# Performance work log

Hardware: AMD Instinct MI355X
Metric: run time of the kernel (lower is better)

The kernel has to match this reference:

```python
import jax, jax.numpy as jnp
import numpy as np
from jax import lax

N_LAYER = 4
D_MODEL = 512
N_HEAD = 8
D_HEAD = 64
D_INNER = 2048
KERNEL = 9
POOL = 8
N_CLASSES = 10
BATCH = 4
RAW_LEN = 8192


def setup_inputs() -> dict:
    key = jax.random.key(0)
    ks = jax.random.split(key, 12)
    s = 0.02
    return {
        "signal": jax.random.normal(ks[0], (BATCH, RAW_LEN), jnp.float32),
        "conv_w": jax.random.normal(ks[1], (KERNEL, 1, D_MODEL), jnp.float32) * s,
        "conv_b": jnp.zeros((D_MODEL,), jnp.float32),
        "qkv_w": jax.random.normal(ks[2], (N_LAYER, D_MODEL, 3 * N_HEAD * D_HEAD), jnp.float32) * s,
        "r_w": jax.random.normal(ks[3], (N_LAYER, D_MODEL, N_HEAD * D_HEAD), jnp.float32) * s,
        "o_w": jax.random.normal(ks[4], (N_LAYER, N_HEAD * D_HEAD, D_MODEL), jnp.float32) * s,
        "ff1_w": jax.random.normal(ks[5], (N_LAYER, D_MODEL, D_INNER), jnp.float32) * s,
        "ff1_b": jnp.zeros((N_LAYER, D_INNER), jnp.float32),
        "ff2_w": jax.random.normal(ks[6], (N_LAYER, D_INNER, D_MODEL), jnp.float32) * s,
        "ff2_b": jnp.zeros((N_LAYER, D_MODEL), jnp.float32),
        "r_w_bias": jax.random.normal(ks[7], (N_HEAD, D_HEAD), jnp.float32) * s,
        "r_r_bias": jax.random.normal(ks[8], (N_HEAD, D_HEAD), jnp.float32) * s,
        "fc_w": jax.random.normal(ks[9], (D_MODEL, N_CLASSES), jnp.float32) * s,
        "fc_b": jnp.zeros((N_CLASSES,), jnp.float32),
    }


def _rel_shift(x):
    # x: [qlen, rlen, bsz, n_head]; TF-XL pad/reshape/slice trick
    q, r, b, n = x.shape
    x = jnp.pad(x, ((0, 0), (1, 0), (0, 0), (0, 0)))
    x = x.reshape(r + 1, q, b, n)[1:]
    return x.reshape(q, r, b, n)


def _forward(signal, conv_w, conv_b, qkv_w, r_w, o_w, ff1_w, ff1_b, ff2_w,
             ff2_b, r_w_bias, r_r_bias, fc_w, fc_b):
    # Conv1D (valid) -> ReLU -> AveragePooling1D
    x = signal[:, :, None]  # [B, L, 1]
    x = lax.conv_general_dilated(x, conv_w, (1,), 'VALID',
                                 dimension_numbers=('NWC', 'WIO', 'NWC')) + conv_b
    x = jax.nn.relu(x)
    B, Lp, D = x.shape
    S = Lp // POOL  # Lp is divisible by POOL for our sizes (keras valid pooling)
    x = x[:, :S * POOL].reshape(B, S, POOL, D).mean(axis=2)
    core = x.transpose(1, 0, 2)  # [S, B, D]

    # sinusoidal relative positional embedding, pos_seq = S-1 .. -(S-1)
    pos_seq = jnp.arange(S - 1, -S, -1, dtype=core.dtype)  # [2S-1]
    inv_freq = 1.0 / (10000.0 ** (jnp.arange(0, D, 2, dtype=core.dtype) / D))
    sin_inp = pos_seq[:, None] * inv_freq[None, :]
    pos_emb = jnp.concatenate([jnp.sin(sin_inp), jnp.cos(sin_inp)], -1)  # [2S-1, D]

    scale = 1.0 / np.sqrt(D_HEAD).astype(np.float32)
    for l in range(N_LAYER):
        heads = core @ qkv_w[l]  # [S, B, 3*H*Dh]
        q, k, v = jnp.split(heads, 3, axis=-1)
        q = q.reshape(S, B, N_HEAD, D_HEAD)
        k = k.reshape(S, B, N_HEAD, D_HEAD)
        v = v.reshape(S, B, N_HEAD, D_HEAD)
        rk = (pos_emb @ r_w[l]).reshape(2 * S - 1, N_HEAD, D_HEAD)

        AC = jnp.einsum('ibnd,jbnd->ijbn', q + r_w_bias, k)      # content term
        BD = jnp.einsum('ibnd,jnd->ijbn', q + r_r_bias, rk)      # position term
        BD = _rel_shift(BD)[:, :S]                                # [S, S, B, H]
        attn_prob = jax.nn.softmax((AC + BD) * scale, axis=1)
        attn_vec = jnp.einsum('ijbn,jbnd->ibnd', attn_prob, v)
        attn_out = attn_vec.reshape(S, B, N_HEAD * D_HEAD) @ o_w[l]
        core = core + attn_out

        # position-wise FF with residual
        h = jax.nn.relu(core @ ff1_w[l] + ff1_b[l]) @ ff2_w[l] + ff2_b[l]
        core = core + h

    # classification head on last timestep
    return core[-1] @ fc_w + fc_b  # [B, n_classes]


def reference(signal, conv_w, conv_b, qkv_w, r_w, o_w, ff1_w, ff1_b, ff2_w,
              ff2_b, r_w_bias, r_r_bias, fc_w, fc_b):
    return _forward(signal, conv_w, conv_b, qkv_w, r_w, o_w, ff1_w, ff1_b,
                    ff2_w, ff2_b, r_w_bias, r_r_bias, fc_w, fc_b)
```

## Files before the change

### kernel.cpp

```cpp
#include <hip/hip_runtime.h>
#include <math.h>

#define S_LEN   1023
#define BATCH_N 4
#define DMODEL  512
#define NHEAD   8
#define DHEAD   64
#define DINNER  2048
#define NLAYER  4
#define RAWLEN  8192
#define POOLW   8
#define KERNW   9
#define RLEN    (2*S_LEN-1)
#define MROWS   (S_LEN*BATCH_N)

using bf16x8 = __attribute__((ext_vector_type(8))) short;
using f32x4  = __attribute__((ext_vector_type(4))) float;

__device__ __forceinline__ unsigned short f2bf(float f) {
    union { float f; unsigned int u; } v; v.f = f;
    unsigned int u = v.u;
    return (unsigned short)((u + 0x7fffu + ((u >> 16) & 1u)) >> 16);
}
__device__ __forceinline__ float bf2f(unsigned short h) {
    union { unsigned int u; float f; } v; v.u = ((unsigned int)h) << 16;
    return v.f;
}

__device__ __forceinline__ void gload_lds16(const void* g, void* l) {
    using gvoid = const __attribute__((address_space(1))) void;
    using lvoid = __attribute__((address_space(3))) void;
    gvoid* gp = reinterpret_cast<gvoid*>(reinterpret_cast<unsigned long long>(g));
    lvoid* lp = reinterpret_cast<lvoid*>((unsigned int)reinterpret_cast<unsigned long long>(l));
    __builtin_amdgcn_global_load_lds(gp, lp, 16, 0, 0);
}

__global__ __launch_bounds__(512) void conv_pool_kernel(
    const float* __restrict__ sig, const float* __restrict__ cw,
    const float* __restrict__ cb, float* __restrict__ core,
    unsigned short* __restrict__ core_bf)
{
    int s = blockIdx.x, b = blockIdx.y, d = threadIdx.x;
    __shared__ float sseg[POOLW + KERNW - 1];
    if (d < POOLW + KERNW - 1) sseg[d] = sig[b*RAWLEN + s*POOLW + d];
    __syncthreads();
    float w[KERNW];
#pragma unroll
    for (int k = 0; k < KERNW; k++) w[k] = cw[k*DMODEL + d];
    float bias = cb[d];
    float acc = 0.f;
#pragma unroll
    for (int p = 0; p < POOLW; p++) {
        float c = bias;
#pragma unroll
        for (int k = 0; k < KERNW; k++) c = fmaf(sseg[p+k], w[k], c);
        acc += fmaxf(c, 0.f);
    }
    float v = acc * (1.0f/POOLW);
    core[(s*BATCH_N + b)*DMODEL + d] = v;
    core_bf[(s*BATCH_N + b)*DMODEL + d] = f2bf(v);
}

__global__ __launch_bounds__(512) void posemb_kernel(unsigned short* __restrict__ pe)
{
    int j = blockIdx.x, d = threadIdx.x;
    float pos = (float)(S_LEN - 1 - j);
    int i = (d < 256) ? d : d - 256;
    float invf = exp2f(-(float)i * (13.287712f/256.0f));
    float a = pos * invf;
    pe[j*DMODEL + d] = f2bf((d < 256) ? __sinf(a) : __cosf(a));
}

__global__ __launch_bounds__(256) void transpose_all_kernel(
    const float* __restrict__ qw, const float* __restrict__ rw,
    const float* __restrict__ ow, const float* __restrict__ f1,
    const float* __restrict__ f2,
    unsigned short* __restrict__ qT, unsigned short* __restrict__ rT,
    unsigned short* __restrict__ oT, unsigned short* __restrict__ f1T,
    unsigned short* __restrict__ f2T)
{
    int id = blockIdx.x;
    const float* W; unsigned short* Wt; int K, N, bx, by;
    if (id < 768)       { W = qw;  Wt = qT;  K = 512;  N = 1536; bx = id % 48; by = id / 48; }
    else if (id < 1024) { id -= 768;  W = rw;  Wt = rT;  K = 512;  N = 512;  bx = id % 16; by = id / 16; }
    else if (id < 1280) { id -= 1024; W = ow;  Wt = oT;  K = 512;  N = 512;  bx = id % 16; by = id / 16; }
    else if (id < 2304) { id -= 1280; W = f1;  Wt = f1T; K = 512;  N = 2048; bx = id % 64; by = id / 64; }
    else                { id -= 2304; W = f2;  Wt = f2T; K = 2048; N = 512;  bx = id % 16; by = id / 16; }

    __shared__ float L[32][33];
    int n0 = bx*32, k0 = by*32;
    int t = threadIdx.x;
    int kk = t>>3, nq = (t&7)*4;
    float4 v = *reinterpret_cast<const float4*>(&W[(size_t)(k0+kk)*N + n0 + nq]);
    L[kk][nq+0]=v.x; L[kk][nq+1]=v.y; L[kk][nq+2]=v.z; L[kk][nq+3]=v.w;
    __syncthreads();
    int nn = t>>3, kq = (t&7)*4;
    ushort4 o;
    o.x = f2bf(L[kq+0][nn]); o.y = f2bf(L[kq+1][nn]);
    o.z = f2bf(L[kq+2][nn]); o.w = f2bf(L[kq+3][nn]);
    *reinterpret_cast<ushort4*>(&Wt[(size_t)(n0+nn)*K + k0 + kq]) = o;
}

template<int BN, bool ACCUM, bool BIAS, bool RELU, bool WF32, bool WBF>
__global__ __launch_bounds__(256) void gemm_mfma(
    const unsigned short* __restrict__ A, const unsigned short* __restrict__ Bt,
    const float* __restrict__ bias, float* __restrict__ C,
    unsigned short* __restrict__ Cb, int M, int N, int K)
{
    constexpr int MF = (BN == 128) ? 4 : 2;
    __shared__ unsigned short As[128*32];
    __shared__ unsigned short Bs[BN*32];
    int bm = blockIdx.y * 128, bn = blockIdx.x * BN;
    int tid = threadIdx.x, lane = tid & 63, wid = tid >> 6;

    f32x4 acc[MF][4];
#pragma unroll
    for (int m=0;m<MF;m++)
#pragma unroll
        for (int n=0;n<4;n++) acc[m][n] = (f32x4){0.f,0.f,0.f,0.f};

    int r0 = wid*16 + (lane>>2);
    int slot = (lane&3)*8;
    int ga0 = bm + r0;      if (ga0 > M-1) ga0 = M-1;
    int ga1 = bm + r0 + 64; if (ga1 > M-1) ga1 = M-1;
    const unsigned short* pA0 = A  + (size_t)ga0*K + slot;
    const unsigned short* pA1 = A  + (size_t)ga1*K + slot;
    const unsigned short* pB0 = Bt + (size_t)(bn + r0)*K + slot;
    const unsigned short* pB1 = (BN==128) ? Bt + (size_t)(bn + r0 + 64)*K + slot : nullptr;
    char* lA0 = (char*)As + wid*1024;
    char* lA1 = (char*)As + (wid+4)*1024;
    char* lB0 = (char*)Bs + wid*1024;
    char* lB1 = (char*)Bs + (wid+4)*1024;

    int ar = (BN==128 ? (wid>>1)*64 : wid*32) + (lane&15);
    int br = (BN==128 ? (wid&1)*64 : 0) + (lane&15);
    int kc = (lane>>4)*8;

    for (int k0 = 0; k0 < K; k0 += 32) {
        __syncthreads();
        gload_lds16(pA0, lA0);
        gload_lds16(pA1, lA1);
        gload_lds16(pB0, lB0);
        if (BN == 128) gload_lds16(pB1, lB1);
        pA0 += 32; pA1 += 32; pB0 += 32; if (BN==128) pB1 += 32;
        __syncthreads();
        bf16x8 a[MF], b[4];
#pragma unroll
        for (int m=0;m<MF;m++) a[m] = *reinterpret_cast<const bf16x8*>(&As[(ar + m*16)*32 + kc]);
#pragma unroll
        for (int n=0;n<4;n++) b[n] = *reinterpret_cast<const bf16x8*>(&Bs[(br + n*16)*32 + kc]);
#pragma unroll
        for (int m=0;m<MF;m++)
#pragma unroll
            for (int n=0;n<4;n++)
                acc[m][n] = __builtin_amdgcn_mfma_f32_16x16x32_bf16(a[m], b[n], acc[m][n], 0,0,0);
    }

    int col0 = bn + (BN==128 ? (wid&1)*64 : 0) + (lane&15);
    int rbase = bm + (BN==128 ? (wid>>1)*64 : wid*32) + (lane>>4)*4;
#pragma unroll
    for (int m=0;m<MF;m++) {
#pragma unroll
        for (int n=0;n<4;n++) {
            int col = col0 + n*16;
            float bv = BIAS ? bias[col] : 0.f;
#pragma unroll
            for (int r=0;r<4;r++) {
                int row = rbase + m*16 + r;
                if (row < M) {
                    float v = acc[m][n][r] + bv;
                    if (RELU) v = fmaxf(v, 0.f);
                    size_t off = (size_t)row*N + col;
                    if (ACCUM) v += C[off];
                    if (WF32) C[off] = v;
                    if (WBF)  Cb[off] = f2bf(v);
                }
            }
        }
    }
}

template<bool ACCUM, bool BIAS, bool RELU, bool WF32, bool WBF>
__global__ __launch_bounds__(256) void gemm_mfma64(
    const unsigned short* __restrict__ A, const unsigned short* __restrict__ Bt,
    const float* __restrict__ bias, float* __restrict__ C,
    unsigned short* __restrict__ Cb, int M, int N, int K)
{
    __shared__ unsigned short As[64*32];
    __shared__ unsigned short Bs[64*32];
    int bm = blockIdx.y * 64, bn = blockIdx.x * 64;
    int tid = threadIdx.x, lane = tid & 63, wid = tid >> 6;
    int wr = wid >> 1, wc = wid & 1;

    f32x4 acc[2][2];
#pragma unroll
    for (int m=0;m<2;m++)
#pragma unroll
        for (int n=0;n<2;n++) acc[m][n] = (f32x4){0.f,0.f,0.f,0.f};

    int r0 = wid*16 + (lane>>2);
    int slot = (lane&3)*8;
    int ga = bm + r0; if (ga > M-1) ga = M-1;
    const unsigned short* pA = A  + (size_t)ga*K + slot;
    const unsigned short* pB = Bt + (size_t)(bn + r0)*K + slot;
    char* lA = (char*)As + wid*1024;
    char* lB = (char*)Bs + wid*1024;

    int ar = wr*32 + (lane&15);
    int br = wc*32 + (lane&15);
    int kc = (lane>>4)*8;

    for (int k0 = 0; k0 < K; k0 += 32) {
        __syncthreads();
        gload_lds16(pA, lA);
        gload_lds16(pB, lB);
        pA += 32; pB += 32;
        __syncthreads();
        bf16x8 a[2], b[2];
#pragma unroll
        for (int m=0;m<2;m++) a[m] = *reinterpret_cast<const bf16x8*>(&As[(ar + m*16)*32 + kc]);
#pragma unroll
        for (int n=0;n<2;n++) b[n] = *reinterpret_cast<const bf16x8*>(&Bs[(br + n*16)*32 + kc]);
#pragma unroll
        for (int m=0;m<2;m++)
#pragma unroll
            for (int n=0;n<2;n++)
                acc[m][n] = __builtin_amdgcn_mfma_f32_16x16x32_bf16(a[m], b[n], acc[m][n], 0,0,0);
    }

    int col0 = bn + wc*32 + (lane&15);
    int rbase = bm + wr*32 + (lane>>4)*4;
#pragma unroll
    for (int m=0;m<2;m++) {
#pragma unroll
        for (int n=0;n<2;n++) {
            int col = col0 + n*16;
            float bv = BIAS ? bias[col] : 0.f;
#pragma unroll
            for (int r=0;r<4;r++) {
                int row = rbase + m*16 + r;
                if (row < M) {
                    float v = acc[m][n][r] + bv;
                    if (RELU) v = fmaxf(v, 0.f);
                    size_t off = (size_t)row*N + col;
                    if (ACCUM) v += C[off];
                    if (WF32) C[off] = v;
                    if (WBF)  Cb[off] = f2bf(v);
                }
            }
        }
    }
}

#define TI 32
#define TJ 32
#define PSTR 40
#define ACSTR 36
#define BDSTR 68

__global__ __launch_bounds__(256) void attn_mfma_kernel(
    const unsigned short* __restrict__ heads,
    const unsigned short* __restrict__ rk,
    const float* __restrict__ rwb, const float* __restrict__ rrb,
    unsigned short* __restrict__ av)
{
    int i0 = blockIdx.x * TI;
    int bn = blockIdx.y; int b = bn >> 3, n = bn & 7;
    int tid = threadIdx.x, lane = tid & 63, wid = tid >> 6;
    int mi = wid >> 1;
    int half = wid & 1;
    int kc = (lane>>4)*8;
    int l15 = lane & 15;

    __shared__ float Sac[TI*ACSTR];
    __shared__ float Sbd[TI*BDSTR];
    __shared__ unsigned short Pb[TI*PSTR];
    __shared__ float mrow[TI], lrow[TI], frow[TI];

    const int base0 = (S_LEN-1) - i0 - (TI-1);

    bf16x8 qwf0, qwf1, qrf0, qrf1;
    {
        int gi = i0 + mi*16 + l15; if (gi > S_LEN-1) gi = S_LEN-1;
        const unsigned short* qb = heads + (size_t)(gi*BATCH_N + b)*1536 + n*64;
        bf16x8 u0 = *reinterpret_cast<const bf16x8*>(qb + kc);
        bf16x8 u1 = *reinterpret_cast<const bf16x8*>(qb + 32 + kc);
#pragma unroll
        for (int e=0;e<8;e++) {
            float f0 = bf2f((unsigned short)u0[e]);
            float f1 = bf2f((unsigned short)u1[e]);
            qwf0[e] = (short)f2bf(f0 + rwb[n*64 + kc + e]);
            qrf0[e] = (short)f2bf(f0 + rrb[n*64 + kc + e]);
            qwf1[e] = (short)f2bf(f1 + rwb[n*64 + 32 + kc + e]);
            qrf1[e] = (short)f2bf(f1 + rrb[n*64 + 32 + kc + e]);
        }
    }
    if (tid < TI) { mrow[tid] = -1e30f; lrow[tid] = 0.f; }

    f32x4 Oa[2];
    Oa[0] = (f32x4){0.f,0.f,0.f,0.f};
    Oa[1] = (f32x4){0.f,0.f,0.f,0.f};

    int rw = mi*16 + (lane>>4)*4;

    for (int t = 0; t < 32; t++) {
        int j0 = t * TJ;
        __syncthreads();

        {
            int gj = j0 + half*16 + l15; if (gj > S_LEN-1) gj = S_LEN-1;
            const unsigned short* kb = heads + (size_t)(gj*BATCH_N + b)*1536 + 512 + n*64;
            bf16x8 kf0 = *reinterpret_cast<const bf16x8*>(kb + kc);
            bf16x8 kf1 = *reinterpret_cast<const bf16x8*>(kb + 32 + kc);
            f32x4 s = (f32x4){0.f,0.f,0.f,0.f};
            s = __builtin_amdgcn_mfma_f32_16x16x32_bf16(qwf0, kf0, s, 0,0,0);
            s = __builtin_amdgcn_mfma_f32_16x16x32_bf16(qwf1, kf1, s, 0,0,0);
            int ci = half*16 + l15;
#pragma unroll
            for (int r=0;r<4;r++) Sac[(rw+r)*ACSTR + ci] = s[r];
        }
        if (t == 0) {
#pragma unroll
            for (int nn=0;nn<2;nn++) {
                int w = (half*2+nn)*16 + l15;
                int gr = base0 + w; gr = gr < 0 ? 0 : (gr > RLEN-1 ? RLEN-1 : gr);
                const unsigned short* rb = rk + (size_t)gr*DMODEL + n*64;
                bf16x8 rf0 = *reinterpret_cast<const bf16x8*>(rb + kc);
                bf16x8 rf1 = *reinterpret_cast<const bf16x8*>(rb + 32 + kc);
                f32x4 sb = (f32x4){0.f,0.f,0.f,0.f};
                sb = __builtin_amdgcn_mfma_f32_16x16x32_bf16(qrf0, rf0, sb, 0,0,0);
                sb = __builtin_amdgcn_mfma_f32_16x16x32_bf16(qrf1, rf1, sb, 0,0,0);
#pragma unroll
                for (int r=0;r<4;r++) Sbd[(rw+r)*BDSTR + w] = sb[r];
            }
        } else {
            int pblk = ((t & 1) ? 0 : 2) + half;
            int w = pblk*16 + l15;
            int off = 32*(t+1) + (w & 31);
            int gr = base0 + off; gr = gr < 0 ? 0 : (gr > RLEN-1 ? RLEN-1 : gr);
            const unsigned short* rb = rk + (size_t)gr*DMODEL + n*64;
            bf16x8 rf0 = *reinterpret_cast<const bf16x8*>(rb + kc);
            bf16x8 rf1 = *reinterpret_cast<const bf16x8*>(rb + 32 + kc);
            f32x4 sb = (f32x4){0.f,0.f,0.f,0.f};
            sb = __builtin_amdgcn_mfma_f32_16x16x32_bf16(qrf0, rf0, sb, 0,0,0);
            sb = __builtin_amdgcn_mfma_f32_16x16x32_bf16(qrf1, rf1, sb, 0,0,0);
#pragma unroll
            for (int r=0;r<4;r++) Sbd[(rw+r)*BDSTR + w] = sb[r];
        }
        __syncthreads();

        {
            int r = tid>>3, seg = tid&7, jl = seg*4;
            float4 ac = *reinterpret_cast<const float4*>(&Sac[r*ACSTR + jl]);
            int cbase = 32*t + (TI-1) - r;
            float s0 = (ac.x + Sbd[r*BDSTR + ((cbase+jl+0)&63)]) * 0.125f;
            float s1 = (ac.y + Sbd[r*BDSTR + ((cbase+jl+1)&63)]) * 0.125f;
            float s2 = (ac.z + Sbd[r*BDSTR + ((cbase+jl+2)&63)]) * 0.125f;
            float s3 = (ac.w + Sbd[r*BDSTR + ((cbase+jl+3)&63)]) * 0.125f;
            int jg = j0 + jl;
            if (jg+0 >= S_LEN) s0 = -1e30f;
            if (jg+1 >= S_LEN) s1 = -1e30f;
            if (jg+2 >= S_LEN) s2 = -1e30f;
            if (jg+3 >= S_LEN) s3 = -1e30f;
            float tm = fmaxf(fmaxf(s0,s1), fmaxf(s2,s3));
            tm = fmaxf(tm, __shfl_xor(tm, 1));
            tm = fmaxf(tm, __shfl_xor(tm, 2));
            tm = fmaxf(tm, __shfl_xor(tm, 4));
            float mo = mrow[r];
            float mnew = fmaxf(mo, tm);
            float f = __expf(mo - mnew);
            float e0 = __expf(s0 - mnew), e1 = __expf(s1 - mnew);
            float e2 = __expf(s2 - mnew), e3 = __expf(s3 - mnew);
            float ssum = e0+e1+e2+e3;
            ssum += __shfl_xor(ssum, 1);
            ssum += __shfl_xor(ssum, 2);
            ssum += __shfl_xor(ssum, 4);
            if (seg == 0) {
                mrow[r] = mnew;
                lrow[r] = lrow[r]*f + ssum;
                frow[r] = f;
            }
            ushort4 pw;
            pw.x = f2bf(e0); pw.y = f2bf(e1); pw.z = f2bf(e2); pw.w = f2bf(e3);
            *reinterpret_cast<ushort4*>(&Pb[r*PSTR + jl]) = pw;
        }
        __syncthreads();

        {
            float f0 = frow[rw+0], f1 = frow[rw+1], f2 = frow[rw+2], f3 = frow[rw+3];
#pragma unroll
            for (int nn=0;nn<2;nn++) {
                Oa[nn][0] *= f0; Oa[nn][1] *= f1; Oa[nn][2] *= f2; Oa[nn][3] *= f3;
            }
            bf16x8 pf = *reinterpret_cast<const bf16x8*>(&Pb[(mi*16 + l15)*PSTR + kc]);
            const unsigned short* vb = heads + 1024 + n*64;
#pragma unroll
            for (int nn=0;nn<2;nn++) {
                int d = (half*2+nn)*16 + l15;
                bf16x8 vf;
#pragma unroll
                for (int e=0;e<8;e++) {
                    int gj = j0 + kc + e; if (gj > S_LEN-1) gj = S_LEN-1;
                    vf[e] = (short)vb[(size_t)(gj*BATCH_N + b)*1536 + d];
                }
                Oa[nn] = __builtin_amdgcn_mfma_f32_16x16x32_bf16(pf, vf, Oa[nn], 0,0,0);
            }
        }
    }
    __syncthreads();

    {
        float linv[4];
#pragma unroll
        for (int r=0;r<4;r++) linv[r] = 1.0f / lrow[rw+r];
#pragma unroll
        for (int nn=0;nn<2;nn++) {
            int d = (half*2+nn)*16 + l15;
#pragma unroll
            for (int r=0;r<4;r++) {
                int gi = i0 + rw + r;
                if (gi < S_LEN)
                    av[(size_t)(gi*BATCH_N + b)*DMODEL + n*64 + d] = f2bf(Oa[nn][r]*linv[r]);
            }
        }
    }
}

__global__ __launch_bounds__(64) void final_kernel(
    const float* __restrict__ core, const float* __restrict__ fcw,
    const float* __restrict__ fcb, float* __restrict__ out)
{
    int idx = blockIdx.x;
    int b = idx / 10, c = idx % 10;
    int lane = threadIdx.x;
    const float* row = &core[(size_t)((S_LEN-1)*BATCH_N + b)*DMODEL];
    float acc = 0.f;
    for (int d = lane; d < DMODEL; d += 64)
        acc = fmaf(row[d], fcw[d*10 + c], acc);
#pragma unroll
    for (int off = 32; off; off >>= 1) acc += __shfl_xor(acc, off);
    if (lane == 0) out[b*10 + c] = acc + fcb[c];
}

extern "C" void kernel_launch(void* const* d_in, const int* in_sizes, int n_in,
                              void* d_out, int out_size, void* d_ws, size_t ws_size,
                              hipStream_t stream)
{
    const float* sig   = (const float*)d_in[0];
    const float* cw    = (const float*)d_in[1];
    const float* cb    = (const float*)d_in[2];
    const float* qkv_w = (const float*)d_in[3];
    const float* r_w   = (const float*)d_in[4];
    const float* o_w   = (const float*)d_in[5];
    const float* ff1_w = (const float*)d_in[6];
    const float* ff1_b = (const float*)d_in[7];
    const float* ff2_w = (const float*)d_in[8];
    const float* ff2_b = (const float*)d_in[9];
    const float* rwb   = (const float*)d_in[10];
    const float* rrb   = (const float*)d_in[11];
    const float* fcw   = (const float*)d_in[12];
    const float* fcb   = (const float*)d_in[13];
    float* out = (float*)d_out;

    float* core = (float*)d_ws;
    unsigned short* core_bf = (unsigned short*)(core + (size_t)MROWS*DMODEL);
    unsigned short* pe_bf   = core_bf + (size_t)MROWS*DMODEL;
    unsigned short* rk_bf   = pe_bf   + (size_t)RLEN*DMODEL;
    unsigned short* av_bf   = rk_bf   + (size_t)RLEN*DMODEL;
    unsigned short* big_bf  = av_bf   + (size_t)MROWS*DMODEL;
    unsigned short* qkvT = big_bf + (size_t)MROWS*DINNER;
    unsigned short* rwT  = qkvT + (size_t)(3*DMODEL)*DMODEL;
    unsigned short* owT  = rwT  + (size_t)DMODEL*DMODEL;
    unsigned short* ff1T = owT  + (size_t)DMODEL*DMODEL;
    unsigned short* ff2T = ff1T + (size_t)DINNER*DMODEL;

    conv_pool_kernel<<<dim3(S_LEN, BATCH_N), 512, 0, stream>>>(sig, cw, cb, core, core_bf);
    posemb_kernel<<<RLEN, 512, 0, stream>>>(pe_bf);

    for (int l = 0; l < NLAYER; l++) {
        transpose_all_kernel<<<3328, 256, 0, stream>>>(
            qkv_w + (size_t)l*DMODEL*(3*DMODEL),
            r_w   + (size_t)l*DMODEL*DMODEL,
            o_w   + (size_t)l*DMODEL*DMODEL,
            ff1_w + (size_t)l*DMODEL*DINNER,
            ff2_w + (size_t)l*DINNER*DMODEL,
            qkvT, rwT, owT, ff1T, ff2T);

        gemm_mfma<64,false,false,false,false,true><<<dim3(24,32), 256, 0, stream>>>(
            core_bf, qkvT, nullptr, nullptr, big_bf, MROWS, 3*DMODEL, DMODEL);
        gemm_mfma64<false,false,false,false,true><<<dim3(8,32), 256, 0, stream>>>(
            pe_bf, rwT, nullptr, nullptr, rk_bf, RLEN, DMODEL, DMODEL);
        attn_mfma_kernel<<<dim3(32,32), 256, 0, stream>>>(big_bf, rk_bf, rwb, rrb, av_bf);
        gemm_mfma64<true,false,false,true,true><<<dim3(8,64), 256, 0, stream>>>(
            av_bf, owT, nullptr, core, core_bf, MROWS, DMODEL, DMODEL);
        gemm_mfma<128,false,true,true,false,true><<<dim3(16,32), 256, 0, stream>>>(
            core_bf, ff1T, ff1_b + (size_t)l*DINNER, nullptr, big_bf, MROWS, DINNER, DMODEL);
        gemm_mfma64<true,true,false,true,true><<<dim3(8,64), 256, 0, stream>>>(
            big_bf, ff2T, ff2_b + (size_t)l*DMODEL, core, core_bf, MROWS, DMODEL, DINNER);
    }

    final_kernel<<<40, 64, 0, stream>>>(core, fcw, fcb, out);
}
```

Before: 729.6 us.

## Double attention key tile width and prefetch V fragments before score phase

The attention kernel now processes 64 key columns per iteration instead of 32, halving the loop trip count and the number of block-wide barriers. The sliding BD window doubles to 128 entries, and the softmax step handles 8 scores per thread. V fragments are gathered from global memory at the top of each iteration, so their latency overlaps with the QK and QR MFMAs and the softmax. This raises register and LDS use per block, which may reduce occupancy.

New measurement: 752.6 us. 3.2% more time.

```diff
diff --git a/kernel.cpp b/kernel.cpp
--- a/kernel.cpp
+++ b/kernel.cpp
@@ -253,10 +253,10 @@
 }
 
 #define TI 32
-#define TJ 32
-#define PSTR 40
-#define ACSTR 36
-#define BDSTR 68
+#define TJ 64
+#define PSTR 72
+#define ACSTR 68
+#define BDSTR 132
 
 __global__ __launch_bounds__(256) void attn_mfma_kernel(
     const unsigned short* __restrict__ heads,
@@ -303,26 +303,45 @@
 
     int rw = mi*16 + (lane>>4)*4;
 
-    for (int t = 0; t < 32; t++) {
+    for (int t = 0; t < 16; t++) {
         int j0 = t * TJ;
         __syncthreads();
 
+        bf16x8 vpre[2][2];
         {
-            int gj = j0 + half*16 + l15; if (gj > S_LEN-1) gj = S_LEN-1;
+            const unsigned short* vb = heads + 1024 + n*64;
+#pragma unroll
+            for (int nn=0;nn<2;nn++) {
+                int d = (half + nn*2)*16 + l15;
+#pragma unroll
+                for (int h=0;h<2;h++) {
+#pragma unroll
+                    for (int e=0;e<8;e++) {
+                        int gj = j0 + h*32 + kc + e; if (gj > S_LEN-1) gj = S_LEN-1;
+                        vpre[nn][h][e] = (short)vb[(size_t)(gj*BATCH_N + b)*1536 + d];
+                    }
+                }
+            }
+        }
+
+#pragma unroll
+        for (int cc=0;cc<2;cc++) {
+            int cb = half + cc*2;
+            int gj = j0 + cb*16 + l15; if (gj > S_LEN-1) gj = S_LEN-1;
             const unsigned short* kb = heads + (size_t)(gj*BATCH_N + b)*1536 + 512 + n*64;
             bf16x8 kf0 = *reinterpret_cast<const bf16x8*>(kb + kc);
             bf16x8 kf1 = *reinterpret_cast<const bf16x8*>(kb + 32 + kc);
             f32x4 s = (f32x4){0.f,0.f,0.f,0.f};
             s = __builtin_amdgcn_mfma_f32_16x16x32_bf16(qwf0, kf0, s, 0,0,0);
             s = __builtin_amdgcn_mfma_f32_16x16x32_bf16(qwf1, kf1, s, 0,0,0);
-            int ci = half*16 + l15;
+            int ci = cb*16 + l15;
 #pragma unroll
             for (int r=0;r<4;r++) Sac[(rw+r)*ACSTR + ci] = s[r];
         }
         if (t == 0) {
 #pragma unroll
-            for (int nn=0;nn<2;nn++) {
-                int w = (half*2+nn)*16 + l15;
+            for (int q=0;q<4;q++) {
+                int w = (half + q*2)*16 + l15;
                 int gr = base0 + w; gr = gr < 0 ? 0 : (gr > RLEN-1 ? RLEN-1 : gr);
                 const unsigned short* rb = rk + (size_t)gr*DMODEL + n*64;
                 bf16x8 rf0 = *reinterpret_cast<const bf16x8*>(rb + kc);
@@ -334,44 +353,49 @@
                 for (int r=0;r<4;r++) Sbd[(rw+r)*BDSTR + w] = sb[r];
             }
         } else {
-            int pblk = ((t & 1) ? 0 : 2) + half;
-            int w = pblk*16 + l15;
-            int off = 32*(t+1) + (w & 31);
-            int gr = base0 + off; gr = gr < 0 ? 0 : (gr > RLEN-1 ? RLEN-1 : gr);
-            const unsigned short* rb = rk + (size_t)gr*DMODEL + n*64;
-            bf16x8 rf0 = *reinterpret_cast<const bf16x8*>(rb + kc);
-            bf16x8 rf1 = *reinterpret_cast<const bf16x8*>(rb + 32 + kc);
-            f32x4 sb = (f32x4){0.f,0.f,0.f,0.f};
-            sb = __builtin_amdgcn_mfma_f32_16x16x32_bf16(qrf0, rf0, sb, 0,0,0);
-            sb = __builtin_amdgcn_mfma_f32_16x16x32_bf16(qrf1, rf1, sb, 0,0,0);
-#pragma unroll
-            for (int r=0;r<4;r++) Sbd[(rw+r)*BDSTR + w] = sb[r];
+            int pbase = (t & 1) ? 0 : 4;
+#pragma unroll
+            for (int q=0;q<2;q++) {
+                int w = (pbase + half + q*2)*16 + l15;
+                int off = 64*(t+1) + (w & 63);
+                int gr = base0 + off; gr = gr < 0 ? 0 : (gr > RLEN-1 ? RLEN-1 : gr);
+                const unsigned short* rb = rk + (size_t)gr*DMODEL + n*64;
+                bf16x8 rf0 = *reinterpret_cast<const bf16x8*>(rb + kc);
+                bf16x8 rf1 = *reinterpret_cast<const bf16x8*>(rb + 32 + kc);
+                f32x4 sb = (f32x4){0.f,0.f,0.f,0.f};
+                sb = __builtin_amdgcn_mfma_f32_16x16x32_bf16(qrf0, rf0, sb, 0,0,0);
+                sb = __builtin_amdgcn_mfma_f32_16x16x32_bf16(qrf1, rf1, sb, 0,0,0);
+#pragma unroll
+                for (int r=0;r<4;r++) Sbd[(rw+r)*BDSTR + w] = sb[r];
+            }
         }
         __syncthreads();
 
         {
-            int r = tid>>3, seg = tid&7, jl = seg*4;
-            float4 ac = *reinterpret_cast<const float4*>(&Sac[r*ACSTR + jl]);
-            int cbase = 32*t + (TI-1) - r;
-            float s0 = (ac.x + Sbd[r*BDSTR + ((cbase+jl+0)&63)]) * 0.125f;
-            float s1 = (ac.y + Sbd[r*BDSTR + ((cbase+jl+1)&63)]) * 0.125f;
-            float s2 = (ac.z + Sbd[r*BDSTR + ((cbase+jl+2)&63)]) * 0.125f;
-            float s3 = (ac.w + Sbd[r*BDSTR + ((cbase+jl+3)&63)]) * 0.125f;
-            int jg = j0 + jl;
-            if (jg+0 >= S_LEN) s0 = -1e30f;
-            if (jg+1 >= S_LEN) s1 = -1e30f;
-            if (jg+2 >= S_LEN) s2 = -1e30f;
-            if (jg+3 >= S_LEN) s3 = -1e30f;
-            float tm = fmaxf(fmaxf(s0,s1), fmaxf(s2,s3));
+            int r = tid>>3, seg = tid&7, jl = seg*8;
+            int cbase = 64*t + (TI-1) - r;
+            float s[8];
+            float4 ac0 = *reinterpret_cast<const float4*>(&Sac[r*ACSTR + jl]);
+            float4 ac1 = *reinterpret_cast<const float4*>(&Sac[r*ACSTR + jl + 4]);
+            s[0]=ac0.x; s[1]=ac0.y; s[2]=ac0.z; s[3]=ac0.w;
+            s[4]=ac1.x; s[5]=ac1.y; s[6]=ac1.z; s[7]=ac1.w;
+#pragma unroll
+            for (int e=0;e<8;e++) {
+                s[e] = (s[e] + Sbd[r*BDSTR + ((cbase+jl+e)&127)]) * 0.125f;
+                if (j0 + jl + e >= S_LEN) s[e] = -1e30f;
+            }
+            float tm = s[0];
+#pragma unroll
+            for (int e=1;e<8;e++) tm = fmaxf(tm, s[e]);
             tm = fmaxf(tm, __shfl_xor(tm, 1));
             tm = fmaxf(tm, __shfl_xor(tm, 2));
             tm = fmaxf(tm, __shfl_xor(tm, 4));
             float mo = mrow[r];
             float mnew = fmaxf(mo, tm);
             float f = __expf(mo - mnew);
-            float e0 = __expf(s0 - mnew), e1 = __expf(s1 - mnew);
-            float e2 = __expf(s2 - mnew), e3 = __expf(s3 - mnew);
-            float ssum = e0+e1+e2+e3;
+            float e0[8], ssum = 0.f;
+#pragma unroll
+            for (int e=0;e<8;e++) { e0[e] = __expf(s[e] - mnew); ssum += e0[e]; }
             ssum += __shfl_xor(ssum, 1);
             ssum += __shfl_xor(ssum, 2);
             ssum += __shfl_xor(ssum, 4);
@@ -380,9 +404,11 @@
                 lrow[r] = lrow[r]*f + ssum;
                 frow[r] = f;
             }
-            ushort4 pw;
-            pw.x = f2bf(e0); pw.y = f2bf(e1); pw.z = f2bf(e2); pw.w = f2bf(e3);
-            *reinterpret_cast<ushort4*>(&Pb[r*PSTR + jl]) = pw;
+            ushort4 pw0, pw1;
+            pw0.x = f2bf(e0[0]); pw0.y = f2bf(e0[1]); pw0.z = f2bf(e0[2]); pw0.w = f2bf(e0[3]);
+            pw1.x = f2bf(e0[4]); pw1.y = f2bf(e0[5]); pw1.z = f2bf(e0[6]); pw1.w = f2bf(e0[7]);
+            *reinterpret_cast<ushort4*>(&Pb[r*PSTR + jl])     = pw0;
+            *reinterpret_cast<ushort4*>(&Pb[r*PSTR + jl + 4]) = pw1;
         }
         __syncthreads();
 
@@ -392,18 +418,12 @@
             for (int nn=0;nn<2;nn++) {
                 Oa[nn][0] *= f0; Oa[nn][1] *= f1; Oa[nn][2] *= f2; Oa[nn][3] *= f3;
             }
-            bf16x8 pf = *reinterpret_cast<const bf16x8*>(&Pb[(mi*16 + l15)*PSTR + kc]);
-            const unsigned short* vb = heads + 1024 + n*64;
+            bf16x8 pf0 = *reinterpret_cast<const bf16x8*>(&Pb[(mi*16 + l15)*PSTR + kc]);
+            bf16x8 pf1 = *reinterpret_cast<const bf16x8*>(&Pb[(mi*16 + l15)*PSTR + 32 + kc]);
 #pragma unroll
             for (int nn=0;nn<2;nn++) {
-                int d = (half*2+nn)*16 + l15;
-                bf16x8 vf;
-#pragma unroll
-                for (int e=0;e<8;e++) {
-                    int gj = j0 + kc + e; if (gj > S_LEN-1) gj = S_LEN-1;
-                    vf[e] = (short)vb[(size_t)(gj*BATCH_N + b)*1536 + d];
-                }
-                Oa[nn] = __builtin_amdgcn_mfma_f32_16x16x32_bf16(pf, vf, Oa[nn], 0,0,0);
+                Oa[nn] = __builtin_amdgcn_mfma_f32_16x16x32_bf16(pf0, vpre[nn][0], Oa[nn], 0,0,0);
+                Oa[nn] = __builtin_amdgcn_mfma_f32_16x16x32_bf16(pf1, vpre[nn][1], Oa[nn], 0,0,0);
             }
         }
     }
@@ -415,7 +435,7 @@
         for (int r=0;r<4;r++) linv[r] = 1.0f / lrow[rw+r];
 #pragma unroll
         for (int nn=0;nn<2;nn++) {
-            int d = (half*2+nn)*16 + l15;
+            int d = (half + nn*2)*16 + l15;
 #pragma unroll
             for (int r=0;r<4;r++) {
                 int gi = i0 + rw + r;
```

## Fuse QKV and rk GEMMs into one launch and pre-transpose V

Applied to the files above, without the earlier changes.

The QKV projection and the positional rk projection now run as one kernel launch, with block columns beyond 24 handling the rk GEMM. A new kernel transposes V per (batch, head) into a contiguous [d, j] layout. The attention PV step can then load each 8-element MFMA operand with a single vector load instead of eight strided scalar gathers. This adds an extra launch plus a V write/read pass per layer. Rows past S_LEN in the transposed V are filled with clamped duplicates, which the zero probabilities in P should cancel.

New measurement: 753.0 us. 3.2% more time.

```diff
diff --git a/kernel.cpp b/kernel.cpp
--- a/kernel.cpp
+++ b/kernel.cpp
@@ -101,16 +101,46 @@
     *reinterpret_cast<ushort4*>(&Wt[(size_t)(n0+nn)*K + k0 + kq]) = o;
 }
 
+__global__ __launch_bounds__(256) void vtrans_kernel(
+    const unsigned short* __restrict__ heads, unsigned short* __restrict__ vt)
+{
+    int j0 = blockIdx.x * 64;
+    int bn = blockIdx.y; int b = bn >> 3, n = bn & 7;
+    __shared__ unsigned short Ls[64*68];
+    int t = threadIdx.x;
+#pragma unroll
+    for (int p = 0; p < 2; p++) {
+        int jr = (t>>3) + p*32, sl = (t&7)*8;
+        int gj = j0 + jr; if (gj > S_LEN-1) gj = S_LEN-1;
+        const unsigned short* src = heads + (size_t)(gj*BATCH_N + b)*1536 + 1024 + n*64 + sl;
+        ushort4 a = *reinterpret_cast<const ushort4*>(src);
+        ushort4 c = *reinterpret_cast<const ushort4*>(src+4);
+        *reinterpret_cast<ushort4*>(&Ls[jr*68 + sl])   = a;
+        *reinterpret_cast<ushort4*>(&Ls[jr*68 + sl+4]) = c;
+    }
+    __syncthreads();
+#pragma unroll
+    for (int p = 0; p < 2; p++) {
+        int d = (t>>3) + p*32, jq = (t&7)*8;
+        ushort4 o0, o1;
+        o0.x = Ls[(jq+0)*68 + d]; o0.y = Ls[(jq+1)*68 + d];
+        o0.z = Ls[(jq+2)*68 + d]; o0.w = Ls[(jq+3)*68 + d];
+        o1.x = Ls[(jq+4)*68 + d]; o1.y = Ls[(jq+5)*68 + d];
+        o1.z = Ls[(jq+6)*68 + d]; o1.w = Ls[(jq+7)*68 + d];
+        unsigned short* dst = vt + ((size_t)bn*64 + d)*1024 + j0 + jq;
+        *reinterpret_cast<ushort4*>(dst) = o0;
+        *reinterpret_cast<ushort4*>(dst+4) = o1;
+    }
+}
+
 template<int BN, bool ACCUM, bool BIAS, bool RELU, bool WF32, bool WBF>
-__global__ __launch_bounds__(256) void gemm_mfma(
+__device__ __forceinline__ void gemm_body(
     const unsigned short* __restrict__ A, const unsigned short* __restrict__ Bt,
     const float* __restrict__ bias, float* __restrict__ C,
-    unsigned short* __restrict__ Cb, int M, int N, int K)
+    unsigned short* __restrict__ Cb, int M, int N, int K, int bm, int bn,
+    unsigned short* As, unsigned short* Bs)
 {
     constexpr int MF = (BN == 128) ? 4 : 2;
-    __shared__ unsigned short As[128*32];
-    __shared__ unsigned short Bs[BN*32];
-    int bm = blockIdx.y * 128, bn = blockIdx.x * BN;
     int tid = threadIdx.x, lane = tid & 63, wid = tid >> 6;
 
     f32x4 acc[MF][4];
@@ -180,6 +210,36 @@
     }
 }
 
+template<int BN, bool ACCUM, bool BIAS, bool RELU, bool WF32, bool WBF>
+__global__ __launch_bounds__(256) void gemm_mfma(
+    const unsigned short* __restrict__ A, const unsigned short* __restrict__ Bt,
+    const float* __restrict__ bias, float* __restrict__ C,
+    unsigned short* __restrict__ Cb, int M, int N, int K)
+{
+    __shared__ unsigned short As[128*32];
+    __shared__ unsigned short Bs[BN*32];
+    gemm_body<BN,ACCUM,BIAS,RELU,WF32,WBF>(A, Bt, bias, C, Cb, M, N, K,
+        blockIdx.y*128, blockIdx.x*BN, As, Bs);
+}
+
+__global__ __launch_bounds__(256) void gemm_qkvrk_kernel(
+    const unsigned short* __restrict__ core_bf, const unsigned short* __restrict__ qkvT,
+    unsigned short* __restrict__ heads,
+    const unsigned short* __restrict__ pe_bf, const unsigned short* __restrict__ rwT,
+    unsigned short* __restrict__ rk_bf)
+{
+    __shared__ unsigned short As[128*32];
+    __shared__ unsigned short Bs[64*32];
+    if (blockIdx.x < 24) {
+        gemm_body<64,false,false,false,false,true>(core_bf, qkvT, nullptr, nullptr, heads,
+            MROWS, 3*DMODEL, DMODEL, blockIdx.y*128, blockIdx.x*64, As, Bs);
+    } else {
+        if (blockIdx.y >= 16) return;
+        gemm_body<64,false,false,false,false,true>(pe_bf, rwT, nullptr, nullptr, rk_bf,
+            RLEN, DMODEL, DMODEL, blockIdx.y*128, (blockIdx.x-24)*64, As, Bs);
+    }
+}
+
 template<bool ACCUM, bool BIAS, bool RELU, bool WF32, bool WBF>
 __global__ __launch_bounds__(256) void gemm_mfma64(
     const unsigned short* __restrict__ A, const unsigned short* __restrict__ Bt,
@@ -261,6 +321,7 @@
 __global__ __launch_bounds__(256) void attn_mfma_kernel(
     const unsigned short* __restrict__ heads,
     const unsigned short* __restrict__ rk,
+    const unsigned short* __restrict__ vt,
     const float* __restrict__ rwb, const float* __restrict__ rrb,
     unsigned short* __restrict__ av)
 {
@@ -302,6 +363,7 @@
     Oa[1] = (f32x4){0.f,0.f,0.f,0.f};
 
     int rw = mi*16 + (lane>>4)*4;
+    const unsigned short* vrow = vt + (size_t)bn*64*1024;
 
     for (int t = 0; t < 32; t++) {
         int j0 = t * TJ;
@@ -393,16 +455,10 @@
                 Oa[nn][0] *= f0; Oa[nn][1] *= f1; Oa[nn][2] *= f2; Oa[nn][3] *= f3;
             }
             bf16x8 pf = *reinterpret_cast<const bf16x8*>(&Pb[(mi*16 + l15)*PSTR + kc]);
-            const unsigned short* vb = heads + 1024 + n*64;
 #pragma unroll
             for (int nn=0;nn<2;nn++) {
                 int d = (half*2+nn)*16 + l15;
-                bf16x8 vf;
-#pragma unroll
-                for (int e=0;e<8;e++) {
-                    int gj = j0 + kc + e; if (gj > S_LEN-1) gj = S_LEN-1;
-                    vf[e] = (short)vb[(size_t)(gj*BATCH_N + b)*1536 + d];
-                }
+                bf16x8 vf = *reinterpret_cast<const bf16x8*>(&vrow[(size_t)d*1024 + j0 + kc]);
                 Oa[nn] = __builtin_amdgcn_mfma_f32_16x16x32_bf16(pf, vf, Oa[nn], 0,0,0);
             }
         }
@@ -473,6 +529,7 @@
     unsigned short* owT  = rwT  + (size_t)DMODEL*DMODEL;
     unsigned short* ff1T = owT  + (size_t)DMODEL*DMODEL;
     unsigned short* ff2T = ff1T + (size_t)DINNER*DMODEL;
+    unsigned short* vt   = ff2T + (size_t)DMODEL*DINNER;
 
     conv_pool_kernel<<<dim3(S_LEN, BATCH_N), 512, 0, stream>>>(sig, cw, cb, core, core_bf);
     posemb_kernel<<<RLEN, 512, 0, stream>>>(pe_bf);
@@ -486,11 +543,10 @@
             ff2_w + (size_t)l*DINNER*DMODEL,
             qkvT, rwT, owT, ff1T, ff2T);
 
-        gemm_mfma<64,false,false,false,false,true><<<dim3(24,32), 256, 0, stream>>>(
-            core_bf, qkvT, nullptr, nullptr, big_bf, MROWS, 3*DMODEL, DMODEL);
-        gemm_mfma64<false,false,false,false,true><<<dim3(8,32), 256, 0, stream>>>(
-            pe_bf, rwT, nullptr, nullptr, rk_bf, RLEN, DMODEL, DMODEL);
-        attn_mfma_kernel<<<dim3(32,32), 256, 0, stream>>>(big_bf, rk_bf, rwb, rrb, av_bf);
+        gemm_qkvrk_kernel<<<dim3(32,32), 256, 0, stream>>>(
+            core_bf, qkvT, big_bf, pe_bf, rwT, rk_bf);
+        vtrans_kernel<<<dim3(16,32), 256, 0, stream>>>(big_bf, vt);
+        attn_mfma_kernel<<<dim3(32,32), 256, 0, stream>>>(big_bf, rk_bf, vt, rwb, rrb, av_bf);
         gemm_mfma64<true,false,false,true,true><<<dim3(8,64), 256, 0, stream>>>(
             av_bf, owT, nullptr, core, core_bf, MROWS, DMODEL, DMODEL);
         gemm_mfma<128,false,true,true,false,true><<<dim3(16,32), 256, 0, stream>>>(
```
